# Performance work log

Measured on AMD Instinct MI355X. Metric: run time of the kernel, lower is better.

## Reference

```python
import jax, jax.numpy as jnp
import numpy as np

N_HEAD = 12

def setup_inputs() -> dict:
    key = jax.random.key(0)
    k1, k2, k3 = jax.random.split(key, 3)
    B, T, C = 4, 2048, 768
    x = jax.random.normal(k1, (B, T, C), dtype=jnp.float32)
    # c_attn params (Linear(n_embd, 3*n_embd)); stored as [in, out] for x @ W
    W_attn = jax.random.normal(k2, (C, 3 * C), dtype=jnp.float32) * (1.0 / np.sqrt(C))
    b_attn = jax.random.normal(k3, (3 * C,), dtype=jnp.float32) * 0.02
    return {"x": x, "W_attn": W_attn, "b_attn": b_attn}

def reference(x, W_attn, b_attn):
    B, T, C = x.shape
    H = N_HEAD
    Dh = C // H
    qkv = x @ W_attn + b_attn                      # [B,T,3C]
    q, k, v = jnp.split(qkv, 3, axis=-1)
    q = q.reshape(B, T, H, Dh)
    k = k.reshape(B, T, H, Dh)
    v = v.reshape(B, T, H, Dh)
    scale = 1.0 / np.sqrt(Dh)
    # scaled QK^T per head: [B,H,T,T]
    scores = jnp.einsum('bqhd,bkhd->bhqk', q * scale, k)
    causal = jnp.tril(jnp.ones((T, T), dtype=bool))  # [T,T]
    # masked-to--inf then ReLU == zero out non-causal and clamp at 0
    p = jnp.where(causal, jnp.maximum(scores, 0.0), 0.0)
    y = jnp.einsum('bhqk,bkhd->bqhd', p, v).reshape(B, T, C)
    return y
```

## Files before the change

kernel.cpp:

```cpp
#include <hip/hip_runtime.h>
#include <cstdint>
#include <cstddef>

typedef unsigned short u16;
typedef unsigned int u32;
typedef __bf16 bf16x8 __attribute__((ext_vector_type(8)));
typedef float f32x4 __attribute__((ext_vector_type(4)));

__device__ __forceinline__ u16 f2bf(float f) {
    unsigned int x = __builtin_bit_cast(unsigned int, f);
    x += 0x7FFFu + ((x >> 16) & 1u);
    return (u16)(x >> 16);
}

__device__ __forceinline__ bf16x8 ldfrag(const u16* p) {
    bf16x8 r;
    __builtin_memcpy(&r, (const u16*)__builtin_assume_aligned(p, 16), 16);
    return r;
}

__device__ __forceinline__ int4 ldg16(const u16* p) {
    int4 r;
    __builtin_memcpy(&r, (const u16*)__builtin_assume_aligned(p, 16), 16);
    return r;
}

__device__ __forceinline__ void async16(u16* lds, const u16* g) {
    __builtin_amdgcn_global_load_lds(
        (const __attribute__((address_space(1))) void*)g,
        (__attribute__((address_space(3))) void*)lds,
        16, 0, 0);
}

__global__ __launch_bounds__(256) void cvt_bf16(const float* __restrict__ in,
                                                u16* __restrict__ out, int n) {
    int i = (blockIdx.x * 256 + threadIdx.x) * 4;
    if (i >= n) return;
    float4 v = *reinterpret_cast<const float4*>(in + i);
    union { u16 e[4]; unsigned long long u; } w;
    w.e[0] = f2bf(v.x); w.e[1] = f2bf(v.y); w.e[2] = f2bf(v.z); w.e[3] = f2bf(v.w);
    *reinterpret_cast<unsigned long long*>(out + i) = w.u;
}

__global__ __launch_bounds__(256) void wt_transpose(const float* __restrict__ W,
                                                    u16* __restrict__ Wt) {
    const int R = 768, Ccols = 2304;
    __shared__ float tile[32][33];
    const int bx = blockIdx.x * 32;
    const int by = blockIdx.y * 32;
    const int tx = threadIdx.x & 31, ty = threadIdx.x >> 5;
    #pragma unroll
    for (int i = 0; i < 32; i += 8)
        tile[ty + i][tx] = W[(size_t)(by + ty + i) * Ccols + bx + tx];
    __syncthreads();
    #pragma unroll
    for (int i = 0; i < 32; i += 8)
        Wt[(size_t)(bx + ty + i) * R + by + tx] = f2bf(tile[tx][ty + i]);
}

__global__ __launch_bounds__(256) void qkv_gemm(const u16* __restrict__ A,
                                                const u16* __restrict__ Bt,
                                                const float* __restrict__ bias,
                                                u16* __restrict__ C) {
    const int N = 2304, K = 768;
    __shared__ __align__(16) u16 sA[128 * 32];
    __shared__ __align__(16) u16 sB[128 * 32];
    const int t = threadIdx.x;
    const int wave = t >> 6, lane = t & 63;
    const int quad = lane >> 4, l16 = lane & 15;
    const int wr = wave >> 1, wc = wave & 1;
    const int m0 = blockIdx.y * 128, n0 = blockIdx.x * 128;

    const int srow = wave * 32 + (lane >> 2);
    const int sseg = lane & 3;

    f32x4 acc[4][4] = {};

    for (int k0 = 0; k0 < K; k0 += 32) {
        __syncthreads();
        #pragma unroll
        for (int j = 0; j < 2; ++j) {
            const int row = srow + j * 16;
            async16(sA + wave * 1024 + j * 512,
                    A + (size_t)(m0 + row) * K + k0 + sseg * 8);
            async16(sB + wave * 1024 + j * 512,
                    Bt + (size_t)(n0 + row) * K + k0 + sseg * 8);
        }
        __syncthreads();

        bf16x8 af[4], bfr[4];
        #pragma unroll
        for (int i = 0; i < 4; ++i)
            af[i] = ldfrag(sA + (wr * 64 + i * 16 + l16) * 32 + quad * 8);
        #pragma unroll
        for (int j = 0; j < 4; ++j)
            bfr[j] = ldfrag(sB + (wc * 64 + j * 16 + l16) * 32 + quad * 8);
        #pragma unroll
        for (int i = 0; i < 4; ++i)
            #pragma unroll
            for (int j = 0; j < 4; ++j)
                acc[i][j] = __builtin_amdgcn_mfma_f32_16x16x32_bf16(af[i], bfr[j], acc[i][j], 0, 0, 0);
    }

    #pragma unroll
    for (int i = 0; i < 4; ++i)
        #pragma unroll
        for (int j = 0; j < 4; ++j) {
            const int col = n0 + wc * 64 + j * 16 + l16;
            const float bc = bias[col];
            const float scale = (col < 768) ? 0.125f : 1.0f;
            #pragma unroll
            for (int r = 0; r < 4; ++r) {
                const int row = m0 + wr * 64 + i * 16 + quad * 4 + r;
                C[(size_t)row * N + col] = f2bf((acc[i][j][r] + bc) * scale);
            }
        }
}

__global__ __launch_bounds__(256) void attn_kernel(const u16* __restrict__ qkv,
                                                   float* __restrict__ out) {
    const int T = 2048, C3 = 2304, Cc = 768, Dh = 64;

    const int bid = blockIdx.x;
    const int rr = bid >> 8;
    const int ss = bid & 255;
    const int x = ss & 15;
    const int qa = (rr == 0) ? x : (rr == 1) ? (15 - x) : ((x + 8) & 15);
    const int qb = 31 - qa;
    const int hb = (ss >> 4) + (rr << 4);
    const int h = hb % 12, b = hb / 12;

    const int t = threadIdx.x;
    const int wave = t >> 6, lane = t & 63;
    const int quad = lane >> 4, l16 = lane & 15;

    __shared__ __align__(16) u16 sK[2][64 * 64];
    __shared__ __align__(16) u32 sVt[2][64 * 36];
    __shared__ __align__(16) u16 sP[4 * 32 * 72];

    const u16* qbase = qkv + (size_t)b * T * C3 + (size_t)h * Dh;
    const u16* kbase = qbase + Cc;
    const u16* vbase = qbase + 2 * Cc;

    bf16x8 aqa0, aqa1, aqb0, aqb1;
    {
        const u16* pa = qbase + (size_t)(qa * 64 + wave * 16 + l16) * C3 + quad * 8;
        const u16* pb = qbase + (size_t)(qb * 64 + wave * 16 + l16) * C3 + quad * 8;
        aqa0 = ldfrag(pa); aqa1 = ldfrag(pa + 32);
        aqb0 = ldfrag(pb); aqb1 = ldfrag(pb + 32);
    }

    f32x4 oa[4] = {}, ob[4] = {};
    u16* myP = sP + wave * (32 * 72);

    const int tp = t & 31, dg = t >> 5;
    const int krow = t >> 3;
    const int kchunk = (t & 7) ^ (krow & 7);

    int4 v0r, v1r;
    auto loadV = [&](int it) {
        const u16* vp = vbase + (size_t)(it * 64 + 2 * tp) * C3 + dg * 8;
        v0r = ldg16(vp);
        v1r = ldg16(vp + C3);
    };
    auto stageK = [&](int it, int bi) {
        const u16* g0 = kbase + (size_t)(it * 64 + krow) * C3 + kchunk * 8;
        const u16* g1 = kbase + (size_t)(it * 64 + 32 + krow) * C3 + kchunk * 8;
        async16(&sK[bi][0] + wave * 512, g0);
        async16(&sK[bi][2048] + wave * 512, g1);
    };
    auto writeV = [&](int bi) {
        union { int4 v; u16 e[8]; } ua, ub;
        ua.v = v0r; ub.v = v1r;
        #pragma unroll
        for (int i = 0; i < 8; ++i)
            sVt[bi][(dg * 8 + i) * 36 + tp] = (u32)ua.e[i] | ((u32)ub.e[i] << 16);
    };

    loadV(0);
    stageK(0, 0);
    writeV(0);
    __syncthreads();

    int buf = 0;
    for (int it = 0; it <= qb; ++it) {
        const bool more = (it < qb);
        if (more) { loadV(it + 1); stageK(it + 1, buf ^ 1); }

        const bool act_a = (it <= qa);
        const bool edge_a = (it == qa), edge_b = (it == qb);
        const u16* sKb = sK[buf];
        const u32* sVb = sVt[buf];

        #pragma unroll
        for (int kt = 0; kt < 4; ++kt) {
            const int tok = kt * 16 + l16;
            const int sw = tok & 7;
            bf16x8 bk0 = ldfrag(sKb + tok * 64 + ((quad ^ sw) << 3));
            bf16x8 bk1 = ldfrag(sKb + tok * 64 + (((quad + 4) ^ sw) << 3));
            {
                f32x4 s = {};
                s = __builtin_amdgcn_mfma_f32_16x16x32_bf16(aqb0, bk0, s, 0, 0, 0);
                s = __builtin_amdgcn_mfma_f32_16x16x32_bf16(aqb1, bk1, s, 0, 0, 0);
                #pragma unroll
                for (int r = 0; r < 4; ++r) {
                    float v = fmaxf(s[r], 0.0f);
                    if (edge_b) {
                        const int qloc = wave * 16 + quad * 4 + r;
                        if (tok > qloc) v = 0.0f;
                    }
                    myP[(16 + quad * 4 + r) * 72 + kt * 16 + l16] = f2bf(v);
                }
            }
            if (act_a) {
                f32x4 s = {};
                s = __builtin_amdgcn_mfma_f32_16x16x32_bf16(aqa0, bk0, s, 0, 0, 0);
                s = __builtin_amdgcn_mfma_f32_16x16x32_bf16(aqa1, bk1, s, 0, 0, 0);
                #pragma unroll
                for (int r = 0; r < 4; ++r) {
                    float v = fmaxf(s[r], 0.0f);
                    if (edge_a) {
                        const int qloc = wave * 16 + quad * 4 + r;
                        if (tok > qloc) v = 0.0f;
                    }
                    myP[(quad * 4 + r) * 72 + kt * 16 + l16] = f2bf(v);
                }
            }
        }

        #pragma unroll
        for (int kk = 0; kk < 2; ++kk) {
            bf16x8 apb = ldfrag(myP + (16 + l16) * 72 + kk * 32 + quad * 8);
            bf16x8 apa;
            if (act_a) apa = ldfrag(myP + l16 * 72 + kk * 32 + quad * 8);
            #pragma unroll
            for (int dt = 0; dt < 4; ++dt) {
                bf16x8 bv = ldfrag((const u16*)(sVb + (dt * 16 + l16) * 36 + kk * 16 + quad * 4));
                ob[dt] = __builtin_amdgcn_mfma_f32_16x16x32_bf16(apb, bv, ob[dt], 0, 0, 0);
                if (act_a)
                    oa[dt] = __builtin_amdgcn_mfma_f32_16x16x32_bf16(apa, bv, oa[dt], 0, 0, 0);
            }
        }

        if (more) writeV(buf ^ 1);
        __syncthreads();
        buf ^= 1;
    }

    #pragma unroll
    for (int dt = 0; dt < 4; ++dt)
        #pragma unroll
        for (int r = 0; r < 4; ++r) {
            const int tga = qa * 64 + wave * 16 + quad * 4 + r;
            const int tgb = qb * 64 + wave * 16 + quad * 4 + r;
            const int c = h * Dh + dt * 16 + l16;
            out[((size_t)b * T + tga) * Cc + c] = oa[dt][r];
            out[((size_t)b * T + tgb) * Cc + c] = ob[dt][r];
        }
}

extern "C" void kernel_launch(void* const* d_in, const int* in_sizes, int n_in,
                              void* d_out, int out_size, void* d_ws, size_t ws_size,
                              hipStream_t stream) {
    const float* x    = (const float*)d_in[0];
    const float* W    = (const float*)d_in[1];
    const float* bias = (const float*)d_in[2];
    float* out = (float*)d_out;

    char* ws = (char*)d_ws;
    const size_t xb_bytes = (size_t)8192 * 768 * 2;
    const size_t wt_bytes = (size_t)2304 * 768 * 2;
    u16* xb  = (u16*)ws;
    u16* Wt  = (u16*)(ws + xb_bytes);
    u16* qkv = (u16*)(ws + xb_bytes + wt_bytes);

    cvt_bf16<<<6144, 256, 0, stream>>>(x, xb, 8192 * 768);
    wt_transpose<<<dim3(72, 24), 256, 0, stream>>>(W, Wt);
    qkv_gemm<<<dim3(18, 64), 256, 0, stream>>>(xb, Wt, bias, qkv);
    attn_kernel<<<768, 256, 0, stream>>>(qkv, out);
}
```

Before: 195.1 us.

## Widen QKV GEMM K-tile with swizzle and share P tile across attention waves

The QKV GEMM now stages a 64-wide K slice per iteration into XOR-swizzled shared memory, halving the number of barrier-separated loop trips and reducing LDS bank conflicts. The attention kernel is reorganised so each wave owns 16 keys and computes transposed scores against all 128 query rows, held in registers. The resulting P tile is written packed into a shared block-wide buffer, adding a barrier before the PV product. It also converts P to bf16 by truncation instead of rounding, and sets launch bounds to request 3 blocks per CU. The aim is less redundant K-fragment loading and better occupancy, at the cost of an extra sync per tile, higher register pressure and slightly lower numerical accuracy.

```diff
diff --git a/kernel.cpp b/kernel.cpp
--- a/kernel.cpp
+++ b/kernel.cpp
@@ -63,43 +63,47 @@
                                                 const float* __restrict__ bias,
                                                 u16* __restrict__ C) {
     const int N = 2304, K = 768;
-    __shared__ __align__(16) u16 sA[128 * 32];
-    __shared__ __align__(16) u16 sB[128 * 32];
+    __shared__ __align__(16) u16 sA[128 * 64];
+    __shared__ __align__(16) u16 sB[128 * 64];
     const int t = threadIdx.x;
     const int wave = t >> 6, lane = t & 63;
     const int quad = lane >> 4, l16 = lane & 15;
     const int wr = wave >> 1, wc = wave & 1;
     const int m0 = blockIdx.y * 128, n0 = blockIdx.x * 128;
 
-    const int srow = wave * 32 + (lane >> 2);
-    const int sseg = lane & 3;
+    const int srow_base = wave * 8 + (lane >> 3);
+    const int schunk = lane & 7;
+    const int swz = (lane >> 3) & 7;
 
     f32x4 acc[4][4] = {};
 
-    for (int k0 = 0; k0 < K; k0 += 32) {
-        __syncthreads();
-        #pragma unroll
-        for (int j = 0; j < 2; ++j) {
-            const int row = srow + j * 16;
-            async16(sA + wave * 1024 + j * 512,
-                    A + (size_t)(m0 + row) * K + k0 + sseg * 8);
-            async16(sB + wave * 1024 + j * 512,
-                    Bt + (size_t)(n0 + row) * K + k0 + sseg * 8);
-        }
-        __syncthreads();
-
-        bf16x8 af[4], bfr[4];
+    for (int k0 = 0; k0 < K; k0 += 64) {
+        __syncthreads();
+        #pragma unroll
+        for (int j = 0; j < 4; ++j) {
+            const int row = j * 32 + srow_base;
+            const int dch = schunk ^ swz;
+            async16(sA + j * 2048 + wave * 512, A + (size_t)(m0 + row) * K + k0 + dch * 8);
+            async16(sB + j * 2048 + wave * 512, Bt + (size_t)(n0 + row) * K + k0 + dch * 8);
+        }
+        __syncthreads();
+
+        bf16x8 af[4][2], bfr[4][2];
+        const int rsw = l16 & 7;
         #pragma unroll
         for (int i = 0; i < 4; ++i)
-            af[i] = ldfrag(sA + (wr * 64 + i * 16 + l16) * 32 + quad * 8);
-        #pragma unroll
-        for (int j = 0; j < 4; ++j)
-            bfr[j] = ldfrag(sB + (wc * 64 + j * 16 + l16) * 32 + quad * 8);
-        #pragma unroll
-        for (int i = 0; i < 4; ++i)
-            #pragma unroll
-            for (int j = 0; j < 4; ++j)
-                acc[i][j] = __builtin_amdgcn_mfma_f32_16x16x32_bf16(af[i], bfr[j], acc[i][j], 0, 0, 0);
+            #pragma unroll
+            for (int h = 0; h < 2; ++h) {
+                af[i][h] = ldfrag(sA + (wr * 64 + i * 16 + l16) * 64 + (((h * 4 + quad) ^ rsw) << 3));
+                bfr[i][h] = ldfrag(sB + (wc * 64 + i * 16 + l16) * 64 + (((h * 4 + quad) ^ rsw) << 3));
+            }
+        #pragma unroll
+        for (int h = 0; h < 2; ++h)
+            #pragma unroll
+            for (int i = 0; i < 4; ++i)
+                #pragma unroll
+                for (int j = 0; j < 4; ++j)
+                    acc[i][j] = __builtin_amdgcn_mfma_f32_16x16x32_bf16(af[i][h], bfr[j][h], acc[i][j], 0, 0, 0);
     }
 
     #pragma unroll
@@ -117,8 +121,8 @@
         }
 }
 
-__global__ __launch_bounds__(256) void attn_kernel(const u16* __restrict__ qkv,
-                                                   float* __restrict__ out) {
+__global__ __launch_bounds__(256, 3) void attn_kernel(const u16* __restrict__ qkv,
+                                                      float* __restrict__ out) {
     const int T = 2048, C3 = 2304, Cc = 768, Dh = 64;
 
     const int bid = blockIdx.x;
@@ -136,26 +140,27 @@
 
     __shared__ __align__(16) u16 sK[2][64 * 64];
     __shared__ __align__(16) u32 sVt[2][64 * 36];
-    __shared__ __align__(16) u16 sP[4 * 32 * 72];
+    __shared__ __align__(16) u16 sP[128 * 72];
 
     const u16* qbase = qkv + (size_t)b * T * C3 + (size_t)h * Dh;
     const u16* kbase = qbase + Cc;
     const u16* vbase = qbase + 2 * Cc;
 
-    bf16x8 aqa0, aqa1, aqb0, aqb1;
-    {
-        const u16* pa = qbase + (size_t)(qa * 64 + wave * 16 + l16) * C3 + quad * 8;
-        const u16* pb = qbase + (size_t)(qb * 64 + wave * 16 + l16) * C3 + quad * 8;
-        aqa0 = ldfrag(pa); aqa1 = ldfrag(pa + 32);
-        aqb0 = ldfrag(pb); aqb1 = ldfrag(pb + 32);
+    bf16x8 qf[8][2];
+    #pragma unroll
+    for (int cg = 0; cg < 8; ++cg) {
+        const int qrow = ((cg < 4) ? qa * 64 : (qb * 64 - 64)) + cg * 16 + l16;
+        const u16* p = qbase + (size_t)qrow * C3 + quad * 8;
+        qf[cg][0] = ldfrag(p);
+        qf[cg][1] = ldfrag(p + 32);
     }
 
-    f32x4 oa[4] = {}, ob[4] = {};
-    u16* myP = sP + wave * (32 * 72);
+    f32x4 oacc[2][4] = {};
 
     const int tp = t & 31, dg = t >> 5;
-    const int krow = t >> 3;
-    const int kchunk = (t & 7) ^ (krow & 7);
+    const int krow_b = wave * 8 + (lane >> 3);
+    const int kswz = (lane >> 3) & 7;
+    const int kch = (lane & 7) ^ kswz;
 
     int4 v0r, v1r;
     auto loadV = [&](int it) {
@@ -164,10 +169,10 @@
         v1r = ldg16(vp + C3);
     };
     auto stageK = [&](int it, int bi) {
-        const u16* g0 = kbase + (size_t)(it * 64 + krow) * C3 + kchunk * 8;
-        const u16* g1 = kbase + (size_t)(it * 64 + 32 + krow) * C3 + kchunk * 8;
-        async16(&sK[bi][0] + wave * 512, g0);
-        async16(&sK[bi][2048] + wave * 512, g1);
+        #pragma unroll
+        for (int j = 0; j < 2; ++j)
+            async16(&sK[bi][0] + j * 2048 + wave * 512,
+                    kbase + (size_t)(it * 64 + j * 32 + krow_b) * C3 + kch * 8);
     };
     auto writeV = [&](int bi) {
         union { int4 v; u16 e[8]; } ua, ub;
@@ -188,57 +193,50 @@
         if (more) { loadV(it + 1); stageK(it + 1, buf ^ 1); }
 
         const bool act_a = (it <= qa);
-        const bool edge_a = (it == qa), edge_b = (it == qb);
-        const u16* sKb = sK[buf];
-        const u32* sVb = sVt[buf];
-
-        #pragma unroll
-        for (int kt = 0; kt < 4; ++kt) {
-            const int tok = kt * 16 + l16;
-            const int sw = tok & 7;
-            bf16x8 bk0 = ldfrag(sKb + tok * 64 + ((quad ^ sw) << 3));
-            bf16x8 bk1 = ldfrag(sKb + tok * 64 + (((quad + 4) ^ sw) << 3));
-            {
-                f32x4 s = {};
-                s = __builtin_amdgcn_mfma_f32_16x16x32_bf16(aqb0, bk0, s, 0, 0, 0);
-                s = __builtin_amdgcn_mfma_f32_16x16x32_bf16(aqb1, bk1, s, 0, 0, 0);
-                #pragma unroll
-                for (int r = 0; r < 4; ++r) {
-                    float v = fmaxf(s[r], 0.0f);
-                    if (edge_b) {
-                        const int qloc = wave * 16 + quad * 4 + r;
-                        if (tok > qloc) v = 0.0f;
-                    }
-                    myP[(16 + quad * 4 + r) * 72 + kt * 16 + l16] = f2bf(v);
-                }
-            }
-            if (act_a) {
-                f32x4 s = {};
-                s = __builtin_amdgcn_mfma_f32_16x16x32_bf16(aqa0, bk0, s, 0, 0, 0);
-                s = __builtin_amdgcn_mfma_f32_16x16x32_bf16(aqa1, bk1, s, 0, 0, 0);
-                #pragma unroll
-                for (int r = 0; r < 4; ++r) {
-                    float v = fmaxf(s[r], 0.0f);
-                    if (edge_a) {
-                        const int qloc = wave * 16 + quad * 4 + r;
-                        if (tok > qloc) v = 0.0f;
-                    }
-                    myP[(quad * 4 + r) * 72 + kt * 16 + l16] = f2bf(v);
-                }
-            }
-        }
-
+
+        bf16x8 kf0, kf1;
+        {
+            const u16* kr = &sK[buf][0] + (wave * 16 + l16) * 64;
+            const int rsw = l16 & 7;
+            kf0 = ldfrag(kr + ((quad ^ rsw) << 3));
+            kf1 = ldfrag(kr + (((quad + 4) ^ rsw) << 3));
+        }
+        const int cg_lo = act_a ? 0 : 4;
+        #pragma unroll
+        for (int cg = 7; cg >= 0; --cg) {
+            if (cg < cg_lo) break;
+            f32x4 s = {};
+            s = __builtin_amdgcn_mfma_f32_16x16x32_bf16(kf0, qf[cg][0], s, 0, 0, 0);
+            s = __builtin_amdgcn_mfma_f32_16x16x32_bf16(kf1, qf[cg][1], s, 0, 0, 0);
+            const bool diag = (cg < 4) ? (it == qa) : (it == qb);
+            u32 bits[4];
+            #pragma unroll
+            for (int r = 0; r < 4; ++r) {
+                float v = fmaxf(s[r], 0.0f);
+                if (diag && (wave * 16 + quad * 4 + r > (cg & 3) * 16 + l16)) v = 0.0f;
+                bits[r] = __builtin_bit_cast(u32, v);
+            }
+            u32 pk[2];
+            pk[0] = (bits[1] & 0xFFFF0000u) | (bits[0] >> 16);
+            pk[1] = (bits[3] & 0xFFFF0000u) | (bits[2] >> 16);
+            __builtin_memcpy((u16*)__builtin_assume_aligned(
+                                 sP + (cg * 16 + l16) * 72 + wave * 16 + quad * 4, 8),
+                             pk, 8);
+        }
+        __syncthreads();
+
+        const u16* sVb = (const u16*)sVt[buf];
         #pragma unroll
         for (int kk = 0; kk < 2; ++kk) {
-            bf16x8 apb = ldfrag(myP + (16 + l16) * 72 + kk * 32 + quad * 8);
-            bf16x8 apa;
-            if (act_a) apa = ldfrag(myP + l16 * 72 + kk * 32 + quad * 8);
+            bf16x8 ap1 = ldfrag(sP + (64 + wave * 16 + l16) * 72 + kk * 32 + quad * 8);
+            bf16x8 ap0;
+            if (act_a) ap0 = ldfrag(sP + (wave * 16 + l16) * 72 + kk * 32 + quad * 8);
             #pragma unroll
             for (int dt = 0; dt < 4; ++dt) {
-                bf16x8 bv = ldfrag((const u16*)(sVb + (dt * 16 + l16) * 36 + kk * 16 + quad * 4));
-                ob[dt] = __builtin_amdgcn_mfma_f32_16x16x32_bf16(apb, bv, ob[dt], 0, 0, 0);
+                bf16x8 bv = ldfrag(sVb + (dt * 16 + l16) * 72 + kk * 32 + quad * 8);
+                oacc[1][dt] = __builtin_amdgcn_mfma_f32_16x16x32_bf16(ap1, bv, oacc[1][dt], 0, 0, 0);
                 if (act_a)
-                    oa[dt] = __builtin_amdgcn_mfma_f32_16x16x32_bf16(apa, bv, oa[dt], 0, 0, 0);
+                    oacc[0][dt] = __builtin_amdgcn_mfma_f32_16x16x32_bf16(ap0, bv, oacc[0][dt], 0, 0, 0);
             }
         }
 
@@ -248,15 +246,15 @@
     }
 
     #pragma unroll
-    for (int dt = 0; dt < 4; ++dt)
-        #pragma unroll
-        for (int r = 0; r < 4; ++r) {
-            const int tga = qa * 64 + wave * 16 + quad * 4 + r;
-            const int tgb = qb * 64 + wave * 16 + quad * 4 + r;
-            const int c = h * Dh + dt * 16 + l16;
-            out[((size_t)b * T + tga) * Cc + c] = oa[dt][r];
-            out[((size_t)b * T + tgb) * Cc + c] = ob[dt][r];
-        }
+    for (int g = 0; g < 2; ++g)
+        #pragma unroll
+        for (int dt = 0; dt < 4; ++dt)
+            #pragma unroll
+            for (int r = 0; r < 4; ++r) {
+                const int tok = (g == 0 ? qa * 64 : qb * 64) + wave * 16 + quad * 4 + r;
+                const int c = h * Dh + dt * 16 + l16;
+                out[((size_t)b * T + tok) * Cc + c] = oacc[g][dt][r];
+            }
 }
 
 extern "C" void kernel_launch(void* const* d_in, const int* in_sizes, int n_in,
```

Result: faster. 186.9 us (-4.2%).
